# Performance work log

Measured on AMD Instinct MI355X. Metric: run time of the kernel, lower is better.

Reference implementation:

```python
import jax, jax.numpy as jnp
import numpy as np

COVERAGE = 0.99
NBINS = 256

def setup_inputs() -> dict:
    key = jax.random.key(0)
    tensor = jax.random.normal(key, (64, 1024, 1024), dtype=jnp.float32)
    return {"tensor": tensor}

def reference(tensor):
    # torch.histogram(tensor, bins=256, min=tensor.min(), max=tensor.max())
    # == jnp.histogram with default range (data min/max), 256 uniform bins.
    flat = tensor.ravel()
    hist, bin_edges = jnp.histogram(flat, bins=NBINS)  # hist: [256], bin_edges: [257]
    cumulative_hist = jnp.cumsum(hist)
    total_count = cumulative_hist[-1]
    # argmax over a bool array returns the index of the first True (as in torch)
    lower_idx = jnp.argmax(cumulative_hist > total_count * (1.0 - COVERAGE) / 2.0)
    upper_idx = jnp.argmax(cumulative_hist > total_count * (1.0 + COVERAGE) / 2.0)
    min_value = bin_edges[lower_idx]
    max_value = bin_edges[upper_idx]
    return (min_value, max_value)
```

## Files before the change

kernel.cpp:

```cpp
#include <hip/hip_runtime.h>

#define NBINS 256
#define NBUCK 4096
#define BSHIFT 20
#define P1BLK 2048
#define NCPY 2
#define CSTRIDE 2049
#define RG 64
#define CG2 2

#define HOFF_W 4096u
#define MOFF_W (HOFF_W + (unsigned)P1BLK * (NBUCK / 2))
#define FOFF_W (MOFF_W + (unsigned)RG * NBUCK)

__device__ __forceinline__ unsigned int f2o(float f) {
    unsigned int u = __float_as_uint(f);
    return (u & 0x80000000u) ? ~u : (u | 0x80000000u);
}
__device__ __forceinline__ float o2f(unsigned int u) {
    unsigned int v = (u & 0x80000000u) ? (u & 0x7fffffffu) : ~u;
    return __uint_as_float(v);
}
__device__ __forceinline__ unsigned int umn(unsigned int a, unsigned int b) { return a < b ? a : b; }
__device__ __forceinline__ unsigned int umx(unsigned int a, unsigned int b) { return a > b ? a : b; }

__global__ void __launch_bounds__(256) hrt_pass1(const float4* __restrict__ in, int n16,
                                                 unsigned int* __restrict__ wsu) {
    __shared__ unsigned int h[NCPY * CSTRIDE];
    for (int i = threadIdx.x; i < NCPY * CSTRIDE; i += 256) h[i] = 0u;
    __syncthreads();
    unsigned int mnu = 0xFFFFFFFFu, mxu = 0u;
    unsigned int cbase = (threadIdx.x & 1u) * CSTRIDE;

#define PROC4(v) { \
    unsigned int u0 = f2o(v.x), u1 = f2o(v.y), u2 = f2o(v.z), u3 = f2o(v.w); \
    mnu = umn(mnu, umn(umn(u0, u1), umn(u2, u3))); \
    mxu = umx(mxu, umx(umx(u0, u1), umx(u2, u3))); \
    unsigned int k0 = u0 >> BSHIFT, k1 = u1 >> BSHIFT, k2 = u2 >> BSHIFT, k3 = u3 >> BSHIFT; \
    atomicAdd(&h[cbase + (k0 >> 1)], (k0 & 1u) ? 0x10000u : 1u); \
    atomicAdd(&h[cbase + (k1 >> 1)], (k1 & 1u) ? 0x10000u : 1u); \
    atomicAdd(&h[cbase + (k2 >> 1)], (k2 & 1u) ? 0x10000u : 1u); \
    atomicAdd(&h[cbase + (k3 >> 1)], (k3 & 1u) ? 0x10000u : 1u); }

    int stride = P1BLK * 256;
    for (int i = blockIdx.x * 256 + threadIdx.x; i < n16; i += stride) {
        float4 v0 = in[4 * i];
        float4 v1 = in[4 * i + 1];
        float4 v2 = in[4 * i + 2];
        float4 v3 = in[4 * i + 3];
        PROC4(v0); PROC4(v1); PROC4(v2); PROC4(v3);
    }
#undef PROC4

    #pragma unroll
    for (int off = 32; off > 0; off >>= 1) {
        mnu = umn(mnu, (unsigned int)__shfl_down((int)mnu, off));
        mxu = umx(mxu, (unsigned int)__shfl_down((int)mxu, off));
    }
    __shared__ unsigned int smn[4], smx[4];
    int lane = threadIdx.x & 63, wid = threadIdx.x >> 6;
    if (lane == 0) { smn[wid] = mnu; smx[wid] = mxu; }
    __syncthreads();
    if (threadIdx.x == 0) {
        #pragma unroll
        for (int w = 1; w < 4; ++w) { mnu = umn(mnu, smn[w]); mxu = umx(mxu, smx[w]); }
        wsu[2 * blockIdx.x]     = mnu;
        wsu[2 * blockIdx.x + 1] = mxu;
    }
    __syncthreads();
    unsigned int* row = wsu + HOFF_W + (unsigned)blockIdx.x * (NBUCK / 2);
    for (int k = threadIdx.x; k < NBUCK / 2; k += 256)
        row[k] = h[k] + h[CSTRIDE + k];
}

__global__ void __launch_bounds__(256) hrt_reduceA(unsigned int* __restrict__ wsu) {
    int rg = blockIdx.x >> 1, cg = blockIdx.x & 1, t = threadIdx.x;
    const uint4* src = (const uint4*)(wsu + HOFF_W);
    unsigned int s[8] = {0, 0, 0, 0, 0, 0, 0, 0};
    int base = cg * 256 + t;
    int r0 = rg * (P1BLK / RG);
    for (int r = r0; r < r0 + P1BLK / RG; ++r) {
        uint4 v = src[r * (NBUCK / 8) + base];
        s[0] += v.x & 0xFFFFu; s[1] += v.x >> 16;
        s[2] += v.y & 0xFFFFu; s[3] += v.y >> 16;
        s[4] += v.z & 0xFFFFu; s[5] += v.z >> 16;
        s[6] += v.w & 0xFFFFu; s[7] += v.w >> 16;
    }
    uint4* dst = (uint4*)(wsu + MOFF_W);
    dst[rg * (NBUCK / 4) + base * 2]     = make_uint4(s[0], s[1], s[2], s[3]);
    dst[rg * (NBUCK / 4) + base * 2 + 1] = make_uint4(s[4], s[5], s[6], s[7]);
}

__global__ void __launch_bounds__(256) hrt_reduceB(unsigned int* __restrict__ wsu) {
    int b = blockIdx.x, t = threadIdx.x;
    const uint4* src = (const uint4*)(wsu + MOFF_W);
    uint4 s = make_uint4(0u, 0u, 0u, 0u);
    int base = b * 256 + t;
    for (int r = 0; r < RG; ++r) {
        uint4 v = src[r * (NBUCK / 4) + base];
        s.x += v.x; s.y += v.y; s.z += v.z; s.w += v.w;
    }
    ((uint4*)(wsu + FOFF_W))[base] = s;
}

__global__ void __launch_bounds__(1024) hrt_finalize(const unsigned int* __restrict__ wsu,
                                                     float* __restrict__ out) {
    __shared__ unsigned int excl[NBUCK + 1];
    __shared__ unsigned int ssum[1024];
    __shared__ unsigned int redmn[16], redmx[16];
    __shared__ float sm[2];
    int t = threadIdx.x;

    unsigned int mnu = 0xFFFFFFFFu, mxu = 0u;
    for (int i = t; i < P1BLK; i += 1024) {
        mnu = umn(mnu, wsu[2 * i]);
        mxu = umx(mxu, wsu[2 * i + 1]);
    }
    #pragma unroll
    for (int off = 32; off > 0; off >>= 1) {
        mnu = umn(mnu, (unsigned int)__shfl_down((int)mnu, off));
        mxu = umx(mxu, (unsigned int)__shfl_down((int)mxu, off));
    }
    int lane = t & 63, wid = t >> 6;
    if (lane == 0) { redmn[wid] = mnu; redmx[wid] = mxu; }

    const uint4* fh = (const uint4*)(wsu + FOFF_W);
    uint4 a = fh[t];
    unsigned int c[4] = { a.x, a.y, a.z, a.w };
    unsigned int s4 = c[0] + c[1] + c[2] + c[3];
    ssum[t] = s4;
    __syncthreads();

    for (int off = 1; off < 1024; off <<= 1) {
        unsigned int v = ssum[t];
        if (t >= off) v += ssum[t - off];
        __syncthreads();
        ssum[t] = v;
        __syncthreads();
    }
    unsigned int run = ssum[t] - s4;
    #pragma unroll
    for (int j = 0; j < 4; ++j) { excl[4 * t + j] = run; run += c[j]; }
    if (t == 1023) excl[NBUCK] = run;

    if (t == 0) {
        unsigned int m1 = 0xFFFFFFFFu, m2 = 0u;
        #pragma unroll
        for (int w = 0; w < 16; ++w) { m1 = umn(m1, redmn[w]); m2 = umx(m2, redmx[w]); }
        sm[0] = o2f(m1); sm[1] = o2f(m2);
    }
    __syncthreads();

    if (t < NBINS) {
        double mn = (double)sm[0], mx = (double)sm[1];
        unsigned int total = excl[NBUCK];
        double delta = (mx - mn) / (double)NBINS;
        double thr0 = (double)total * ((1.0 - 0.99) / 2.0);
        double thr1 = (double)total * ((1.0 + 0.99) / 2.0);

        auto estcum = [&](double e) -> double {
            unsigned int u = f2o((float)e);
            unsigned int k = u >> BSHIFT;
            unsigned int lou = k << BSHIFT;
            unsigned int hiu = (k == NBUCK - 1) ? 0xFFFFFFFFu : ((k + 1) << BSHIFT);
            double flo = (double)o2f(lou), fhi = (double)o2f(hiu);
            double fr = (e - flo) / (fhi - flo);
            fr = fr < 0.0 ? 0.0 : (fr > 1.0 ? 1.0 : fr);
            double cl = (double)excl[k], ch = (double)excl[k + 1];
            return cl + (ch - cl) * fr;
        };

        double c_hi = estcum(mn + (double)(t + 1) * delta);
        double c_lo = estcum(mn + (double)t * delta);
        if (c_hi > thr0 && !(c_lo > thr0)) out[0] = (float)(mn + (double)t * delta);
        if (c_hi > thr1 && !(c_lo > thr1)) out[1] = (float)(mn + (double)t * delta);
    }
}

extern "C" void kernel_launch(void* const* d_in, const int* in_sizes, int n_in,
                              void* d_out, int out_size, void* d_ws, size_t ws_size,
                              hipStream_t stream) {
    const float4* in = (const float4*)d_in[0];
    int n = in_sizes[0];
    int n16 = n / 16;
    unsigned int* wsu = (unsigned int*)d_ws;
    float* out = (float*)d_out;

    hrt_pass1<<<P1BLK, 256, 0, stream>>>(in, n16, wsu);
    hrt_reduceA<<<RG * CG2, 256, 0, stream>>>(wsu);
    hrt_reduceB<<<4, 256, 0, stream>>>(wsu);
    hrt_finalize<<<1, 1024, 0, stream>>>(wsu, out);
}
```

Before: 62.16 us.

## Merge two-stage histogram reduction into one kernel with in-block tree reduce

Result: slower. 65.27 us (+5.0%).

```diff
diff --git a/kernel.cpp b/kernel.cpp
--- a/kernel.cpp
+++ b/kernel.cpp
@@ -6,12 +6,9 @@
 #define P1BLK 2048
 #define NCPY 2
 #define CSTRIDE 2049
-#define RG 64
-#define CG2 2
 
 #define HOFF_W 4096u
-#define MOFF_W (HOFF_W + (unsigned)P1BLK * (NBUCK / 2))
-#define FOFF_W (MOFF_W + (unsigned)RG * NBUCK)
+#define FOFF_W (HOFF_W + (unsigned)P1BLK * (NBUCK / 2))
 
 __device__ __forceinline__ unsigned int f2o(float f) {
     unsigned int u = __float_as_uint(f);
@@ -73,34 +70,31 @@
         row[k] = h[k] + h[CSTRIDE + k];
 }
 
-__global__ void __launch_bounds__(256) hrt_reduceA(unsigned int* __restrict__ wsu) {
-    int rg = blockIdx.x >> 1, cg = blockIdx.x & 1, t = threadIdx.x;
-    const uint4* src = (const uint4*)(wsu + HOFF_W);
-    unsigned int s[8] = {0, 0, 0, 0, 0, 0, 0, 0};
-    int base = cg * 256 + t;
-    int r0 = rg * (P1BLK / RG);
-    for (int r = r0; r < r0 + P1BLK / RG; ++r) {
-        uint4 v = src[r * (NBUCK / 8) + base];
-        s[0] += v.x & 0xFFFFu; s[1] += v.x >> 16;
-        s[2] += v.y & 0xFFFFu; s[3] += v.y >> 16;
-        s[4] += v.z & 0xFFFFu; s[5] += v.z >> 16;
-        s[6] += v.w & 0xFFFFu; s[7] += v.w >> 16;
+__global__ void __launch_bounds__(256) hrt_reduce(unsigned int* __restrict__ wsu) {
+    __shared__ unsigned int slo[256], shi[256];
+    int t = threadIdx.x;
+    int wl = t & 7;
+    int r0 = t >> 3;
+    unsigned int w = (unsigned)blockIdx.x * 8 + wl;
+    const unsigned int* src = wsu + HOFF_W + w;
+    unsigned int lo = 0, hi = 0;
+    for (int r = r0; r < P1BLK; r += 32) {
+        unsigned int v = src[(unsigned)r * (NBUCK / 2)];
+        lo += v & 0xFFFFu;
+        hi += v >> 16;
     }
-    uint4* dst = (uint4*)(wsu + MOFF_W);
-    dst[rg * (NBUCK / 4) + base * 2]     = make_uint4(s[0], s[1], s[2], s[3]);
-    dst[rg * (NBUCK / 4) + base * 2 + 1] = make_uint4(s[4], s[5], s[6], s[7]);
-}
-
-__global__ void __launch_bounds__(256) hrt_reduceB(unsigned int* __restrict__ wsu) {
-    int b = blockIdx.x, t = threadIdx.x;
-    const uint4* src = (const uint4*)(wsu + MOFF_W);
-    uint4 s = make_uint4(0u, 0u, 0u, 0u);
-    int base = b * 256 + t;
-    for (int r = 0; r < RG; ++r) {
-        uint4 v = src[r * (NBUCK / 4) + base];
-        s.x += v.x; s.y += v.y; s.z += v.z; s.w += v.w;
+    slo[t] = lo; shi[t] = hi;
+    __syncthreads();
+    #pragma unroll
+    for (int off = 128; off >= 8; off >>= 1) {
+        if (t < off) { slo[t] += slo[t + off]; shi[t] += shi[t + off]; }
+        __syncthreads();
     }
-    ((uint4*)(wsu + FOFF_W))[base] = s;
+    if (t < 8) {
+        unsigned int ww = (unsigned)blockIdx.x * 8 + t;
+        wsu[FOFF_W + 2 * ww]     = slo[t];
+        wsu[FOFF_W + 2 * ww + 1] = shi[t];
+    }
 }
 
 __global__ void __launch_bounds__(1024) hrt_finalize(const unsigned int* __restrict__ wsu,
@@ -187,7 +181,6 @@
     float* out = (float*)d_out;
 
     hrt_pass1<<<P1BLK, 256, 0, stream>>>(in, n16, wsu);
-    hrt_reduceA<<<RG * CG2, 256, 0, stream>>>(wsu);
-    hrt_reduceB<<<4, 256, 0, stream>>>(wsu);
+    hrt_reduce<<<256, 256, 0, stream>>>(wsu);
     hrt_finalize<<<1, 1024, 0, stream>>>(wsu, out);
 }
```
